# Performance work log

Measured on AMD Instinct MI355X. Metric: run time of the kernel, lower is better.

The kernel has to match this reference:

```python
import jax, jax.numpy as jnp
import numpy as np

B, D, K, L = 16384, 255, 4, 16  # batch, destinations, tunnels/dst, outgoing links
T = D * K                        # total tunnels = 1020
EPS = 1e-8


def setup_inputs() -> dict:
    key = jax.random.key(0)
    k1, k2, k3, k4, k5 = jax.random.split(key, 5)
    pred_ratios = jax.random.uniform(k1, (B, T), dtype=jnp.float32)
    demands = jax.random.uniform(k2, (B, D), dtype=jnp.float32) * 100.0
    current_link_utils = jax.random.uniform(k3, (B, L), dtype=jnp.float32)
    link_capacities = jax.random.uniform(k4, (L,), dtype=jnp.float32) * 900.0 + 100.0
    tunnel_to_link = jax.random.randint(k5, (T,), 0, L, dtype=jnp.int32)
    return {
        "pred_ratios": pred_ratios,
        "demands": demands,
        "current_link_utils": current_link_utils,
        "link_capacities": link_capacities,
        "tunnel_to_link": tunnel_to_link,
    }


def reference(pred_ratios, demands, current_link_utils, link_capacities, tunnel_to_link):
    # Equal group sizes: destination d owns tunnels [d*K, (d+1)*K)
    Tn = pred_ratios.shape[1]
    Dn = demands.shape[1]
    Kn = Tn // Dn
    Ln = link_capacities.shape[0]
    # tunnel_traffic[b, t] = demand[b, dst(t)] * ratio[b, t]
    tunnel_traffic = pred_ratios * jnp.repeat(demands, Kn, axis=1)  # [B, T]
    # scatter-add tunnels into links, expressed as a dense [T, L] one-hot GEMM
    onehot = jax.nn.one_hot(tunnel_to_link, Ln, dtype=pred_ratios.dtype)  # [T, L]
    node_link_traffic = tunnel_traffic @ onehot  # [B, L]
    node_link_util = node_link_traffic / (link_capacities[None, :] + EPS)
    variance_loss = jnp.var(node_link_util, axis=1, ddof=1).mean()  # torch.var is unbiased
    congestion_penalty = (node_link_util * current_link_utils).sum(axis=1).mean()
    max_util_loss = node_link_util.max(axis=1).mean()
    return 0.3 * variance_loss + 0.5 * congestion_penalty + 0.2 * max_util_loss
```

## Files before the change

### kernel.cpp

```cpp
#include <hip/hip_runtime.h>

constexpr int T_TUN = 1020;
constexpr int D_DST = 255;
constexpr int L_LNK = 16;
constexpr float EPS = 1e-8f;
constexpr int ROWS_PER_BLOCK = 8;

__device__ __forceinline__ float read_lane_f(float v, int l) {
  return __builtin_bit_cast(float,
      __builtin_amdgcn_readlane(__builtin_bit_cast(int, v), l));
}

__global__ __launch_bounds__(256) void rowloss_kernel(
    const float* __restrict__ pred,
    const float* __restrict__ demands,
    const float* __restrict__ cur,
    const float* __restrict__ caps,
    const int*   __restrict__ t2l,
    float* __restrict__ out, float invB)
{
  const int tid  = threadIdx.x;
  const int lane = tid & 63;
  const int w    = tid >> 6;

  __shared__ float priv_all[4][2][64 * L_LNK];
  __shared__ float wacc[4];

  const int b16 = lane & 15;
  const int g   = lane >> 4;
  const float capinv = 1.0f / (caps[b16] + EPS);

  int off[4][4];
  bool dv[4];
#pragma unroll
  for (int j = 0; j < 4; ++j) {
    const int d = lane + 64 * j;
    dv[j] = (d < D_DST);
    const int dd = dv[j] ? d : 0;
    const int4 lk = ((const int4*)t2l)[dd];
    off[j][0] = (lk.x * 64 + lane) & 1023;
    off[j][1] = (lk.y * 64 + lane) & 1023;
    off[j][2] = (lk.z * 64 + lane) & 1023;
    off[j][3] = (lk.w * 64 + lane) & 1023;
  }

  const int row0 = blockIdx.x * ROWS_PER_BLOCK + w * 2;

  float4 r4[2][4];
  float  dm[2][4];
  float  mycur[2];
#pragma unroll
  for (int r = 0; r < 2; ++r) {
    const int b = row0 + r;
    const float4* prow = (const float4*)(pred + (size_t)b * T_TUN);
    const float*  drow = demands + (size_t)b * D_DST;
    mycur[r] = cur[(size_t)b * L_LNK + b16];
#pragma unroll
    for (int j = 0; j < 4; ++j) {
      const int d = lane + 64 * j;
      if (dv[j]) { r4[r][j] = prow[d]; dm[r][j] = drow[d]; }
    }
  }

  {
    const float4 z = make_float4(0.f, 0.f, 0.f, 0.f);
#pragma unroll
    for (int r = 0; r < 2; ++r) {
      float4* pz = (float4*)priv_all[w][r];
#pragma unroll
      for (int i = 0; i < 4; ++i) pz[lane + 64 * i] = z;
    }
  }

#pragma unroll
  for (int j = 0; j < 4; ++j) {
    if (!dv[j]) continue;
#pragma unroll
    for (int r = 0; r < 2; ++r) {
      const float4 v = r4[r][j];
      const float  d = dm[r][j];
      priv_all[w][r][off[j][0]] += v.x * d;
      priv_all[w][r][off[j][1]] += v.y * d;
      priv_all[w][r][off[j][2]] += v.z * d;
      priv_all[w][r][off[j][3]] += v.w * d;
    }
  }

  const int rbase = b16 * 64 + g * 16;
  float acc = 0.0f;
  float cs[2] = {0.0f, 0.0f};
#pragma unroll
  for (int k = 0; k < 16; ++k) {
    const int idx = (rbase + ((k + b16) & 15)) & 1023;
#pragma unroll
    for (int r = 0; r < 2; ++r) cs[r] += priv_all[w][r][idx];
  }
#pragma unroll
  for (int r = 0; r < 2; ++r) {
    cs[r] += __shfl_xor(cs[r], 16, 64);
    cs[r] += __shfl_xor(cs[r], 32, 64);
  }

  float val[2];
#pragma unroll
  for (int r = 0; r < 2; ++r) {
    const float u = cs[r] * capinv;
    val[r] = (g == 0) ? u : (g == 1) ? (u * u) : (g == 2) ? (u * mycur[r]) : u;
  }
#pragma unroll
  for (int m = 1; m < 16; m <<= 1) {
#pragma unroll
    for (int r = 0; r < 2; ++r) {
      const float o  = __shfl_xor(val[r], m, 64);
      const float sm = val[r] + o;
      const float mm = fmaxf(val[r], o);
      val[r] = (g == 3) ? mm : sm;
    }
  }
#pragma unroll
  for (int r = 0; r < 2; ++r) {
    const float s1 = read_lane_f(val[r], 0);
    const float s2 = read_lane_f(val[r], 16);
    const float s3 = read_lane_f(val[r], 32);
    const float mx = read_lane_f(val[r], 48);
    const float var = (s2 - s1 * s1 * (1.0f / 16.0f)) * (1.0f / 15.0f);
    acc += 0.3f * var + 0.5f * s3 + 0.2f * mx;
  }

  if (lane == 0) wacc[w] = acc;
  __syncthreads();
  if (tid == 0) atomicAdd(out, (wacc[0] + wacc[1] + wacc[2] + wacc[3]) * invB);
}

__global__ void zero_out_kernel(float* __restrict__ out) { out[0] = 0.0f; }

extern "C" void kernel_launch(void* const* d_in, const int* in_sizes, int n_in,
                              void* d_out, int out_size, void* d_ws, size_t ws_size,
                              hipStream_t stream) {
  const float* pred    = (const float*)d_in[0];
  const float* demands = (const float*)d_in[1];
  const float* cur     = (const float*)d_in[2];
  const float* caps    = (const float*)d_in[3];
  const int*   t2l     = (const int*)d_in[4];
  float* out = (float*)d_out;

  const int L = in_sizes[3];
  const int B = in_sizes[2] / L;

  const int grid = B / ROWS_PER_BLOCK;

  zero_out_kernel<<<1, 1, 0, stream>>>(out);
  rowloss_kernel<<<grid, 256, 0, stream>>>(pred, demands, cur, caps, t2l,
                                           out, 1.0f / (float)B);
}
```

Measured before the change: 122.9 us.

## Interleave two rows' link bins as float2 and drop block-level barrier

Each wave now keeps its two rows' private link bins interleaved as float2 cells. Every tunnel update becomes one 64-bit LDS read-modify-write covering both rows instead of two 32-bit ones, which halves the LDS instruction count for the scatter and for the readback. The per-block shared reduction and __syncthreads are removed, so each wave issues its own atomicAdd. That costs four times as many global atomics to the single output word in exchange for dropping the barrier.

```diff
diff --git a/kernel.cpp b/kernel.cpp
--- a/kernel.cpp
+++ b/kernel.cpp
@@ -23,8 +23,8 @@
   const int lane = tid & 63;
   const int w    = tid >> 6;
 
-  __shared__ float priv_all[4][2][64 * L_LNK];
-  __shared__ float wacc[4];
+  __shared__ float2 bins_all[4][L_LNK][64];
+  float2 (*binsw)[64] = bins_all[w];
 
   const int b16 = lane & 15;
   const int g   = lane >> 4;
@@ -38,10 +38,10 @@
     dv[j] = (d < D_DST);
     const int dd = dv[j] ? d : 0;
     const int4 lk = ((const int4*)t2l)[dd];
-    off[j][0] = (lk.x * 64 + lane) & 1023;
-    off[j][1] = (lk.y * 64 + lane) & 1023;
-    off[j][2] = (lk.z * 64 + lane) & 1023;
-    off[j][3] = (lk.w * 64 + lane) & 1023;
+    off[j][0] = lk.x * 64 + lane;
+    off[j][1] = lk.y * 64 + lane;
+    off[j][2] = lk.z * 64 + lane;
+    off[j][3] = lk.w * 64 + lane;
   }
 
   const int row0 = blockIdx.x * ROWS_PER_BLOCK + w * 2;
@@ -64,48 +64,44 @@
 
   {
     const float4 z = make_float4(0.f, 0.f, 0.f, 0.f);
+    float4* pz = (float4*)binsw;
 #pragma unroll
-    for (int r = 0; r < 2; ++r) {
-      float4* pz = (float4*)priv_all[w][r];
-#pragma unroll
-      for (int i = 0; i < 4; ++i) pz[lane + 64 * i] = z;
-    }
+    for (int i = 0; i < 8; ++i) pz[lane + 64 * i] = z;
   }
 
+  float2* cells = (float2*)binsw;
 #pragma unroll
   for (int j = 0; j < 4; ++j) {
     if (!dv[j]) continue;
 #pragma unroll
-    for (int r = 0; r < 2; ++r) {
-      const float4 v = r4[r][j];
-      const float  d = dm[r][j];
-      priv_all[w][r][off[j][0]] += v.x * d;
-      priv_all[w][r][off[j][1]] += v.y * d;
-      priv_all[w][r][off[j][2]] += v.z * d;
-      priv_all[w][r][off[j][3]] += v.w * d;
+    for (int c = 0; c < 4; ++c) {
+      const float rx = (c == 0) ? r4[0][j].x : (c == 1) ? r4[0][j].y
+                     : (c == 2) ? r4[0][j].z : r4[0][j].w;
+      const float ry = (c == 0) ? r4[1][j].x : (c == 1) ? r4[1][j].y
+                     : (c == 2) ? r4[1][j].z : r4[1][j].w;
+      float2 v = cells[off[j][c]];
+      v.x += rx * dm[0][j];
+      v.y += ry * dm[1][j];
+      cells[off[j][c]] = v;
     }
   }
 
-  const int rbase = b16 * 64 + g * 16;
-  float acc = 0.0f;
-  float cs[2] = {0.0f, 0.0f};
+  float csx = 0.0f, csy = 0.0f;
 #pragma unroll
   for (int k = 0; k < 16; ++k) {
-    const int idx = (rbase + ((k + b16) & 15)) & 1023;
-#pragma unroll
-    for (int r = 0; r < 2; ++r) cs[r] += priv_all[w][r][idx];
+    const int copy = 16 * g + ((k + b16) & 15);
+    const float2 v = binsw[b16][copy];
+    csx += v.x; csy += v.y;
   }
-#pragma unroll
-  for (int r = 0; r < 2; ++r) {
-    cs[r] += __shfl_xor(cs[r], 16, 64);
-    cs[r] += __shfl_xor(cs[r], 32, 64);
-  }
+  csx += __shfl_xor(csx, 16, 64); csx += __shfl_xor(csx, 32, 64);
+  csy += __shfl_xor(csy, 16, 64); csy += __shfl_xor(csy, 32, 64);
 
   float val[2];
-#pragma unroll
-  for (int r = 0; r < 2; ++r) {
-    const float u = cs[r] * capinv;
-    val[r] = (g == 0) ? u : (g == 1) ? (u * u) : (g == 2) ? (u * mycur[r]) : u;
+  {
+    const float u0 = csx * capinv;
+    const float u1 = csy * capinv;
+    val[0] = (g == 0) ? u0 : (g == 1) ? (u0 * u0) : (g == 2) ? (u0 * mycur[0]) : u0;
+    val[1] = (g == 0) ? u1 : (g == 1) ? (u1 * u1) : (g == 2) ? (u1 * mycur[1]) : u1;
   }
 #pragma unroll
   for (int m = 1; m < 16; m <<= 1) {
@@ -117,6 +113,8 @@
       val[r] = (g == 3) ? mm : sm;
     }
   }
+
+  float acc = 0.0f;
 #pragma unroll
   for (int r = 0; r < 2; ++r) {
     const float s1 = read_lane_f(val[r], 0);
@@ -127,9 +125,7 @@
     acc += 0.3f * var + 0.5f * s3 + 0.2f * mx;
   }
 
-  if (lane == 0) wacc[w] = acc;
-  __syncthreads();
-  if (tid == 0) atomicAdd(out, (wacc[0] + wacc[1] + wacc[2] + wacc[3]) * invB);
+  if (lane == 0) atomicAdd(out, acc * invB);
 }
 
 __global__ void zero_out_kernel(float* __restrict__ out) { out[0] = 0.0f; }
```

Result: slower. 200.9 us (+63.5%).
